# Kernel tuning notes

Hardware: AMD Instinct MI355X
Metric: run time of the kernel (lower is better)

Reference implementation:

```python
import jax, jax.numpy as jnp
import numpy as np

N_NODES = 50000
N_EDGES = 800000
IN_CH = 64
OUT_CH = 32
HEADS = 4
NUM_EDGE_TYPES = 64


def _sincos_pe(max_len, d_model):
    pos = np.arange(max_len, dtype=np.float32)[:, None]
    div = np.exp(np.arange(0, d_model, 2, dtype=np.float32) * (-np.log(10000.0) / d_model))
    pe = np.zeros((max_len, d_model), dtype=np.float32)
    pe[:, 0::2] = np.sin(pos * div)
    pe[:, 1::2] = np.cos(pos * div)
    return jnp.asarray(pe)


def setup_inputs() -> dict:
    key = jax.random.key(0)
    k1, k2, k3, k4, k5, k6 = jax.random.split(key, 6)
    x = jax.random.uniform(k1, (N_NODES, IN_CH), dtype=jnp.float32)
    edge_index = jax.random.randint(k2, (2, N_EDGES), 0, N_NODES, dtype=jnp.int64)
    edge_type = jax.random.randint(k3, (N_EDGES,), 0, NUM_EDGE_TYPES, dtype=jnp.int64)
    pe = _sincos_pe(NUM_EDGE_TYPES, IN_CH)
    W = jax.random.normal(k4, (IN_CH, HEADS * OUT_CH), dtype=jnp.float32) * 0.1
    att_src = jax.random.normal(k5, (HEADS, OUT_CH), dtype=jnp.float32) * 0.1
    att_dst = jax.random.normal(k6, (HEADS, OUT_CH), dtype=jnp.float32) * 0.1
    bias = jnp.zeros((HEADS * OUT_CH,), dtype=jnp.float32)
    return {"x": x, "edge_index": edge_index, "edge_type": edge_type, "pe": pe,
            "W": W, "att_src": att_src, "att_dst": att_dst, "bias": bias}


def reference(x, edge_index, edge_type, pe, W, att_src, att_dst, bias):
    N = x.shape[0]
    H, C = att_src.shape
    src, dst = edge_index[0], edge_index[1]

    # edge-wise positional encoding scatter-added into source nodes
    x_pos = x.at[src].add(pe[edge_type])

    # GATConv (PyG defaults: add_self_loops=True, negative_slope=0.2, concat=True)
    xl = (x_pos @ W).reshape(N, H, C)              # [N, H, C]
    a_src = (xl * att_src[None]).sum(-1)           # [N, H]
    a_dst = (xl * att_dst[None]).sum(-1)           # [N, H]

    self_idx = jnp.arange(N)
    src2 = jnp.concatenate([src, self_idx])        # [E'] with self loops
    dst2 = jnp.concatenate([dst, self_idx])

    alpha = jax.nn.leaky_relu(a_src[src2] + a_dst[dst2], 0.2)   # [E', H]
    amax = jax.ops.segment_max(alpha, dst2, num_segments=N)     # per-target max
    ex = jnp.exp(alpha - amax[dst2])
    denom = jax.ops.segment_sum(ex, dst2, num_segments=N)
    coef = ex / denom[dst2]                                     # segment softmax

    out = jax.ops.segment_sum(coef[:, :, None] * xl[src2], dst2, num_segments=N)
    out = out.reshape(N, H * C) + bias
    return jax.nn.elu(out)
```

## Files before the change

### kernel.cpp

```cpp
#include <hip/hip_runtime.h>
#include <cstdint>
#include <cstddef>

#define N_NODES 50000
#define N_EDGES 800000
#define IN_CH   64
#define OC      128
#define HEADS   4
#define CH      32

#define NB      391
#define BCAP    2560
#define EPB     2048
#define HIST_BLOCKS ((N_EDGES + EPB - 1) / EPB)

#define SENTINEL N_NODES
#define LST_LEN  (N_EDGES + 4 * N_NODES)

typedef __attribute__((ext_vector_type(8))) short short8;
typedef __attribute__((ext_vector_type(4))) float f32x4;

static inline int ceil_div(int a, int b){ return (a + b - 1) / b; }

__device__ __forceinline__ float lrelu(float x){ return fmaxf(x, 0.2f * x); }

__device__ __forceinline__ float bf_lo(unsigned u){ return __uint_as_float(u << 16); }
__device__ __forceinline__ float bf_hi(unsigned u){ return __uint_as_float(u & 0xFFFF0000u); }

__device__ __forceinline__ unsigned pack_bf16(float x, float y){
  unsigned ux = __float_as_uint(x), uy = __float_as_uint(y);
  ux += 0x7FFFu + ((ux >> 16) & 1u);
  uy += 0x7FFFu + ((uy >> 16) & 1u);
  return (ux >> 16) | (uy & 0xFFFF0000u);
}

__global__ __launch_bounds__(256) void k_histA(const int* __restrict__ ei,
                                               const int* __restrict__ et,
                                               int* __restrict__ btail,
                                               unsigned* __restrict__ bbuf){
  __shared__ int cnt[784];
  __shared__ int lofs[784];
  __shared__ int gpos[784];
  __shared__ unsigned stage[2 * EPB];
  __shared__ int sred[256];
  int tid = threadIdx.x;
  for (int i = tid; i < 784; i += 256) cnt[i] = 0;
  __syncthreads();

  int e0 = blockIdx.x * EPB;
  unsigned ent[16];
  int rnk[16];
  short bck[16];
  #pragma unroll
  for (int j = 0; j < 8; ++j){
    int e = e0 + j * 256 + tid;
    bck[2 * j] = -1; bck[2 * j + 1] = -1;
    if (e < N_EDGES){
      int s = ei[e], d = ei[N_EDGES + e], t = et[e];
      int bd = d >> 7, bs = s >> 7;
      ent[2 * j]     = ((unsigned)bd << 23) | ((unsigned)(d & 127) << 16) | (unsigned)s;
      ent[2 * j + 1] = ((unsigned)bs << 23) | ((unsigned)(s & 127) << 16) | (unsigned)t;
      bck[2 * j]     = (short)bd;
      bck[2 * j + 1] = (short)(391 + bs);
      rnk[2 * j]     = atomicAdd(&cnt[bd], 1);
      rnk[2 * j + 1] = atomicAdd(&cnt[391 + bs], 1);
    }
  }
  __syncthreads();

  int v[4], pre[4], run = 0;
  #pragma unroll
  for (int i = 0; i < 4; ++i){
    int idx = tid * 4 + i;
    v[i] = (idx < 784) ? cnt[idx] : 0;
    pre[i] = run; run += v[i];
  }
  sred[tid] = run; __syncthreads();
  for (int off = 1; off < 256; off <<= 1){
    int t = (tid >= off) ? sred[tid - off] : 0;
    __syncthreads();
    sred[tid] += t;
    __syncthreads();
  }
  int toff = sred[tid] - run;
  #pragma unroll
  for (int i = 0; i < 4; ++i){
    int idx = tid * 4 + i;
    if (idx < 784) lofs[idx] = toff + pre[i];
  }
  __syncthreads();

  #pragma unroll
  for (int j = 0; j < 16; ++j){
    if (bck[j] >= 0) stage[lofs[bck[j]] + rnk[j]] = ent[j];
  }
  for (int b = tid; b < 782; b += 256){
    int c = cnt[b];
    gpos[b] = c ? atomicAdd(&btail[b], c) : 0;
  }
  __syncthreads();

  int totalD = lofs[391];
  int totalA = lofs[782];
  for (int i = tid; i < totalA; i += 256){
    unsigned e = stage[i];
    int b9 = (int)(e >> 23);
    int bc = (i < totalD) ? b9 : 391 + b9;
    int gp = gpos[bc] + (i - lofs[bc]);
    if (gp < BCAP) bbuf[(size_t)bc * BCAP + gp] = e;
  }
}

__global__ __launch_bounds__(256) void k_passB(const unsigned* __restrict__ bbuf,
                                               const int* __restrict__ btail,
                                               int* __restrict__ row_dst,
                                               unsigned short* __restrict__ lst,
                                               unsigned* __restrict__ cb){
  int g = blockIdx.x, tid = threadIdx.x;
  if (g < NB){
    __shared__ int cnt[128], sc[128], cur[128], red[256];
    __shared__ int sbase;
    int d0 = g << 7;
    int nn = min(128, N_NODES - d0);
    int cnt_b = min(btail[g], BCAP);
    int part = 0;
    for (int q = tid; q < g; q += 256) part += min(btail[q], BCAP);
    red[tid] = part; __syncthreads();
    for (int off = 128; off > 0; off >>= 1){
      if (tid < off) red[tid] += red[tid + off];
      __syncthreads();
    }
    if (tid == 0) sbase = red[0];
    if (tid < 128) cnt[tid] = 0;
    __syncthreads();
    int base0 = sbase + 4 * d0;
    for (int i = tid; i < cnt_b; i += 256)
      atomicAdd(&cnt[(bbuf[(size_t)g * BCAP + i] >> 16) & 127], 1);
    __syncthreads();
    if (tid < 128) sc[tid] = cnt[tid];
    __syncthreads();
    for (int off = 1; off < 128; off <<= 1){
      int t = (tid < 128 && tid >= off) ? sc[tid - off] : 0;
      __syncthreads();
      if (tid < 128) sc[tid] += t;
      __syncthreads();
    }
    if (tid < nn){
      int ex = sc[tid] - cnt[tid];
      cur[tid] = ex + 4 * tid;
      row_dst[d0 + tid] = base0 + ex + 4 * tid;
    }
    if (g == NB - 1 && tid == 0) row_dst[N_NODES] = base0 + cnt_b + 4 * nn;
    __syncthreads();
    for (int i = tid; i < cnt_b; i += 256){
      unsigned e = bbuf[(size_t)g * BCAP + i];
      int p = atomicAdd(&cur[(e >> 16) & 127], 1);
      lst[base0 + p] = (unsigned short)(e & 0xFFFFu);
    }
    __syncthreads();
    if (tid < nn){
      int pe_ = cur[tid];
      #pragma unroll
      for (int k = 0; k < 4; ++k) lst[base0 + pe_ + k] = (unsigned short)SENTINEL;
    }
  } else {
    __shared__ unsigned hist[128 * 16];
    int n0 = (g - NB) << 7;
    int nn = min(128, N_NODES - n0);
    for (int i = tid; i < 2048; i += 256) hist[i] = 0;
    __syncthreads();
    int cnt_b = min(btail[g], BCAP);
    for (int i = tid; i < cnt_b; i += 256){
      unsigned e = bbuf[(size_t)g * BCAP + i];
      unsigned t = e & 63u;
      atomicAdd(&hist[((e >> 16) & 127) * 16 + (t >> 2)], 1u << (8 * (t & 3)));
    }
    __syncthreads();
    for (int o = tid; o < 4096; o += 256){
      int i = o >> 5, j = o & 31;
      if (i < nn){
        unsigned w = hist[i * 16 + (j >> 1)];
        unsigned sh = 16 * (j & 1);
        cb[(size_t)(n0 + i) * 32 + j] =
          pack_bf16((float)((w >> sh) & 0xFFu), (float)((w >> (sh + 8)) & 0xFFu));
      }
    }
  }
}

__global__ __launch_bounds__(256) void k_prep(const float* __restrict__ pe,
                                              const float* __restrict__ W,
                                              unsigned* __restrict__ Bh,
                                              int* __restrict__ btail,
                                              float* __restrict__ a_src,
                                              unsigned* __restrict__ xh,
                                              unsigned short* __restrict__ lst){
  __shared__ float sPe[64 * 64];
  __shared__ float sW64[64 * 16];
  __shared__ float sPeW[64 * 16];
  int tid = threadIdx.x;
  int nt = blockIdx.x;
  int n0 = nt * 16;
  if (nt == 0){
    for (int i = tid; i < 1024; i += 256) btail[i] = 0;
    if (tid < 64) xh[(size_t)SENTINEL * 64 + tid] = 0;
    if (tid < 4)  a_src[SENTINEL * 4 + tid] = -1e30f;
    if (tid < 32) lst[LST_LEN + tid] = (unsigned short)SENTINEL;
  }
  for (int i = tid; i < 1024; i += 256)
    ((float4*)sPe)[i] = ((const float4*)pe)[i];
  for (int i = tid; i < 1024; i += 256){
    int k = i >> 4, j = i & 15;
    sW64[i] = W[k * 128 + n0 + j];
  }
  __syncthreads();
  for (int i = tid; i < 1024; i += 256){
    int t = i >> 4, j = i & 15;
    float a = 0.f;
    #pragma unroll
    for (int k = 0; k < 64; ++k) a += sPe[t * 64 + k] * sW64[k * 16 + j];
    sPeW[i] = a;
  }
  __syncthreads();
  for (int m = tid; m < 1024; m += 256){
    int j2 = m & 3, l = (m >> 2) & 63, kk = m >> 8;
    int k = kk * 32 + (l >> 4) * 8 + 2 * j2;
    int jl = l & 15;
    float v0, v1;
    if (k < 64){ v0 = sW64[k * 16 + jl]; v1 = sW64[(k + 1) * 16 + jl]; }
    else       { v0 = sPeW[(k - 64) * 16 + jl]; v1 = sPeW[(k - 63) * 16 + jl]; }
    Bh[nt * 1024 + m] = pack_bf16(v0, v1);
  }
}

#define GEMM_ROWS 64
__global__ __launch_bounds__(256) void k_gemm_mfma(const float* __restrict__ x,
                                                   const unsigned* __restrict__ cb,
                                                   const unsigned* __restrict__ Bh,
                                                   const float* __restrict__ att_s,
                                                   const float* __restrict__ att_d,
                                                   float* __restrict__ a_src,
                                                   float* __restrict__ a_dst,
                                                   unsigned* __restrict__ xh){
  __shared__ unsigned sA[4096];
  __shared__ unsigned sB[8192];
  int tid = threadIdx.x;
  int row0 = blockIdx.x * GEMM_ROWS;

  {
    const uint4* srcp = (const uint4*)Bh;
    uint4* dstp = (uint4*)sB;
    #pragma unroll
    for (int i = 0; i < 8; ++i) dstp[tid + i * 256] = srcp[tid + i * 256];
  }
  {
    int r = tid >> 2, q = tid & 3;
    int n = row0 + r;
    unsigned swz = (unsigned)((r & 7) << 4);
    float4 xv[4];
    if (n < N_NODES){
      const float4* xr = (const float4*)(x + (size_t)n * 64);
      #pragma unroll
      for (int i = 0; i < 4; ++i) xv[i] = xr[q * 4 + i];
    } else {
      #pragma unroll
      for (int i = 0; i < 4; ++i) xv[i] = make_float4(0.f, 0.f, 0.f, 0.f);
    }
    unsigned pk[8];
    #pragma unroll
    for (int i = 0; i < 4; ++i){
      pk[2 * i]     = pack_bf16(xv[i].x, xv[i].y);
      pk[2 * i + 1] = pack_bf16(xv[i].z, xv[i].w);
    }
    unsigned b0 = (unsigned)(r * 256 + q * 32);
    *(uint4*)(sA + (((b0)      ^ swz) >> 2)) = make_uint4(pk[0], pk[1], pk[2], pk[3]);
    *(uint4*)(sA + (((b0 + 16) ^ swz) >> 2)) = make_uint4(pk[4], pk[5], pk[6], pk[7]);
    uint4 c0, c1;
    if (n < N_NODES){
      const uint4* cr = (const uint4*)(cb + (size_t)n * 32);
      c0 = cr[q * 2]; c1 = cr[q * 2 + 1];
    } else {
      c0 = make_uint4(0, 0, 0, 0); c1 = c0;
    }
    unsigned b1 = (unsigned)(r * 256 + 128 + q * 32);
    *(uint4*)(sA + (((b1)      ^ swz) >> 2)) = c0;
    *(uint4*)(sA + (((b1 + 16) ^ swz) >> 2)) = c1;
  }
  __syncthreads();

  int wid = tid >> 6, l = tid & 63;
  int c15 = l & 15, kq = l >> 4;
  int arow = wid * 16 + c15;
  f32x4 acc[8];
  #pragma unroll
  for (int nt = 0; nt < 8; ++nt) acc[nt] = (f32x4){0.f, 0.f, 0.f, 0.f};

  #pragma unroll
  for (int kk = 0; kk < 4; ++kk){
    unsigned abyte = (unsigned)(arow * 256 + kk * 64 + kq * 16);
    abyte ^= (unsigned)((arow & 7) << 4);
    short8 af = *(const short8*)((const char*)sA + abyte);
    #pragma unroll
    for (int nt = 0; nt < 8; ++nt){
      short8 bf = *(const short8*)(sB + (size_t)((nt * 4 + kk) * 64 + l) * 4);
      acc[nt] = __builtin_amdgcn_mfma_f32_16x16x32_bf16(af, bf, acc[nt], 0, 0, 0);
    }
  }

  float asv[8], adv[8];
  #pragma unroll
  for (int nt = 0; nt < 8; ++nt){
    asv[nt] = att_s[nt * 16 + c15];
    adv[nt] = att_d[nt * 16 + c15];
  }
  #pragma unroll
  for (int r = 0; r < 4; ++r){
    int row = row0 + wid * 16 + kq * 4 + r;
    bool valid = row < N_NODES;
    #pragma unroll
    for (int h = 0; h < 4; ++h){
      float ps = acc[2 * h][r] * asv[2 * h] + acc[2 * h + 1][r] * asv[2 * h + 1];
      float pd = acc[2 * h][r] * adv[2 * h] + acc[2 * h + 1][r] * adv[2 * h + 1];
      #pragma unroll
      for (int m = 1; m < 16; m <<= 1){
        ps += __shfl_xor(ps, m);
        pd += __shfl_xor(pd, m);
      }
      if (valid && c15 == 0){
        a_src[row * 4 + h] = ps;
        a_dst[row * 4 + h] = pd;
      }
    }
    #pragma unroll
    for (int nt = 0; nt < 8; ++nt){
      float own = acc[nt][r];
      float nb = __shfl_xor(own, 1);
      if (valid && !(c15 & 1))
        xh[(size_t)row * 64 + nt * 8 + (c15 >> 1)] = pack_bf16(own, nb);
    }
  }
}

__global__ __launch_bounds__(256) void k_aggregate(const int* __restrict__ row_dst,
                                                   const unsigned short* __restrict__ lst,
                                                   const float* __restrict__ a_src,
                                                   const float* __restrict__ a_dst,
                                                   const unsigned* __restrict__ xh,
                                                   const float* __restrict__ bias,
                                                   float* __restrict__ out){
  int n = (blockIdx.x * blockDim.x + threadIdx.x) >> 6;
  if (n >= N_NODES) return;
  int l = threadIdx.x & 63;
  int h = l >> 4;
  float ad = a_dst[n * 4 + h];

  float w = __expf(lrelu(a_src[n * 4 + h] + ad));
  unsigned uv = xh[(size_t)n * 64 + l];
  float l0 = w, l1 = 0.f, l2 = 0.f, l3 = 0.f;
  float a0x = w * bf_lo(uv), a0y = w * bf_hi(uv);
  float a1x = 0.f, a1y = 0.f, a2x = 0.f, a2y = 0.f, a3x = 0.f, a3y = 0.f;

  int k0 = row_dst[n];
  int k1 = row_dst[n + 1] - 4;

  int sA = (int)lst[k0], sB = (int)lst[k0 + 1], sC = (int)lst[k0 + 2], sD = (int)lst[k0 + 3];
  unsigned uA = xh[(size_t)sA * 64 + l]; float bA = a_src[sA * 4 + h];
  unsigned uB = xh[(size_t)sB * 64 + l]; float bB = a_src[sB * 4 + h];
  unsigned uC = xh[(size_t)sC * 64 + l]; float bC = a_src[sC * 4 + h];
  unsigned uD = xh[(size_t)sD * 64 + l]; float bD = a_src[sD * 4 + h];

  for (int j = k0; j < k1; j += 4){
    int nsA = (int)lst[j + 4], nsB = (int)lst[j + 5];
    int nsC = (int)lst[j + 6], nsD = (int)lst[j + 7];
    unsigned nuA = xh[(size_t)nsA * 64 + l]; float nbA = a_src[nsA * 4 + h];
    unsigned nuB = xh[(size_t)nsB * 64 + l]; float nbB = a_src[nsB * 4 + h];
    unsigned nuC = xh[(size_t)nsC * 64 + l]; float nbC = a_src[nsC * 4 + h];
    unsigned nuD = xh[(size_t)nsD * 64 + l]; float nbD = a_src[nsD * 4 + h];
    float wA = __expf(lrelu(bA + ad));
    l0 += wA;
    a0x = fmaf(wA, bf_lo(uA), a0x); a0y = fmaf(wA, bf_hi(uA), a0y);
    float wB = __expf(lrelu(bB + ad));
    l1 += wB;
    a1x = fmaf(wB, bf_lo(uB), a1x); a1y = fmaf(wB, bf_hi(uB), a1y);
    float wC = __expf(lrelu(bC + ad));
    l2 += wC;
    a2x = fmaf(wC, bf_lo(uC), a2x); a2y = fmaf(wC, bf_hi(uC), a2y);
    float wD = __expf(lrelu(bD + ad));
    l3 += wD;
    a3x = fmaf(wD, bf_lo(uD), a3x); a3y = fmaf(wD, bf_hi(uD), a3y);
    uA = nuA; bA = nbA; uB = nuB; bB = nbB;
    uC = nuC; bC = nbC; uD = nuD; bD = nbD;
  }
  float lsum = (l0 + l1) + (l2 + l3);
  float accx = (a0x + a1x) + (a2x + a3x);
  float accy = (a0y + a1y) + (a2y + a3y);
  float2 b = ((const float2*)bias)[l];
  float r0 = accx / lsum + b.x;
  float r1 = accy / lsum + b.y;
  float2 o;
  o.x = r0 > 0.f ? r0 : expm1f(r0);
  o.y = r1 > 0.f ? r1 : expm1f(r1);
  ((float2*)out)[(size_t)n * 64 + l] = o;
}

extern "C" void kernel_launch(void* const* d_in, const int* in_sizes, int n_in,
                              void* d_out, int out_size, void* d_ws, size_t ws_size,
                              hipStream_t stream){
  const float* x     = (const float*)d_in[0];
  const int*   ei    = (const int*)d_in[1];
  const int*   et    = (const int*)d_in[2];
  const float* pe    = (const float*)d_in[3];
  const float* W     = (const float*)d_in[4];
  const float* att_s = (const float*)d_in[5];
  const float* att_d = (const float*)d_in[6];
  const float* bias  = (const float*)d_in[7];
  float* out = (float*)d_out;

  int*      btail   = (int*)d_ws;
  int*      row_dst = btail + 1024;
  unsigned* Bh      = (unsigned*)(row_dst + N_NODES + 8);
  unsigned* cb      = Bh + 8192;
  float*    a_src   = (float*)(cb + (size_t)N_NODES * 32);
  float*    a_dst   = a_src + (size_t)(N_NODES + 1) * 4;
  unsigned* xh      = (unsigned*)(a_dst + (size_t)N_NODES * 4);
  unsigned* bbuf    = xh + (size_t)(N_NODES + 1) * 64;
  unsigned short* lst = (unsigned short*)(bbuf + (size_t)2 * NB * BCAP);

  const int B = 256;

  k_prep<<<8, B, 0, stream>>>(pe, W, Bh, btail, a_src, xh, lst);
  k_histA<<<HIST_BLOCKS, B, 0, stream>>>(ei, et, btail, bbuf);
  k_passB<<<2 * NB, B, 0, stream>>>(bbuf, btail, row_dst, lst, cb);
  k_gemm_mfma<<<ceil_div(N_NODES, GEMM_ROWS), B, 0, stream>>>(x, cb, Bh,
                                                              att_s, att_d,
                                                              a_src, a_dst, xh);
  k_aggregate<<<ceil_div(N_NODES * 64, B), B, 0, stream>>>(row_dst, lst, a_src, a_dst,
                                                           xh, bias, out);
}
```

Before: 105.5 us.

## Fuse edge-type histogram and MFMA GEMM into passB source-bucket blocks

The source-bucket half of k_passB now runs the bf16 MFMA projection directly from its shared-memory edge-type histogram, in two 64-row halves per 128-node bucket. This drops the cb count matrix round trip through global memory and the separate k_gemm_mfma launch. In exchange, those blocks use much more shared memory (about 56KB), which may lower occupancy, and they now do the GEMM serially after the histogram.

```diff
diff --git a/kernel.cpp b/kernel.cpp
--- a/kernel.cpp
+++ b/kernel.cpp
@@ -115,7 +115,13 @@
                                                const int* __restrict__ btail,
                                                int* __restrict__ row_dst,
                                                unsigned short* __restrict__ lst,
-                                               unsigned* __restrict__ cb){
+                                               const float* __restrict__ x,
+                                               const unsigned* __restrict__ Bh,
+                                               const float* __restrict__ att_s,
+                                               const float* __restrict__ att_d,
+                                               float* __restrict__ a_src,
+                                               float* __restrict__ a_dst,
+                                               unsigned* __restrict__ xh){
   int g = blockIdx.x, tid = threadIdx.x;
   if (g < NB){
     __shared__ int cnt[128], sc[128], cur[128], red[256];
@@ -165,8 +171,9 @@
     }
   } else {
     __shared__ unsigned hist[128 * 16];
+    __shared__ unsigned sB[8192];
+    __shared__ unsigned sA[4096];
     int n0 = (g - NB) << 7;
-    int nn = min(128, N_NODES - n0);
     for (int i = tid; i < 2048; i += 256) hist[i] = 0;
     __syncthreads();
     int cnt_b = min(btail[g], BCAP);
@@ -175,15 +182,106 @@
       unsigned t = e & 63u;
       atomicAdd(&hist[((e >> 16) & 127) * 16 + (t >> 2)], 1u << (8 * (t & 3)));
     }
-    __syncthreads();
-    for (int o = tid; o < 4096; o += 256){
-      int i = o >> 5, j = o & 31;
-      if (i < nn){
-        unsigned w = hist[i * 16 + (j >> 1)];
-        unsigned sh = 16 * (j & 1);
-        cb[(size_t)(n0 + i) * 32 + j] =
-          pack_bf16((float)((w >> sh) & 0xFFu), (float)((w >> (sh + 8)) & 0xFFu));
+    {
+      const uint4* srcp = (const uint4*)Bh;
+      uint4* dstp = (uint4*)sB;
+      #pragma unroll
+      for (int i = 0; i < 8; ++i) dstp[tid + i * 256] = srcp[tid + i * 256];
+    }
+    __syncthreads();
+
+    int wid = tid >> 6, l = tid & 63;
+    int c15 = l & 15, kq = l >> 4;
+    float asv[8], adv[8];
+    #pragma unroll
+    for (int nt = 0; nt < 8; ++nt){
+      asv[nt] = att_s[nt * 16 + c15];
+      adv[nt] = att_d[nt * 16 + c15];
+    }
+
+    for (int half = 0; half < 2; ++half){
+      int row0 = n0 + half * 64;
+      {
+        int r = tid >> 2, q = tid & 3;
+        int n = row0 + r;
+        unsigned swz = (unsigned)((r & 7) << 4);
+        float4 xv[4];
+        if (n < N_NODES){
+          const float4* xr = (const float4*)(x + (size_t)n * 64);
+          #pragma unroll
+          for (int i = 0; i < 4; ++i) xv[i] = xr[q * 4 + i];
+        } else {
+          #pragma unroll
+          for (int i = 0; i < 4; ++i) xv[i] = make_float4(0.f, 0.f, 0.f, 0.f);
+        }
+        unsigned pk[8];
+        #pragma unroll
+        for (int i = 0; i < 4; ++i){
+          pk[2 * i]     = pack_bf16(xv[i].x, xv[i].y);
+          pk[2 * i + 1] = pack_bf16(xv[i].z, xv[i].w);
+        }
+        unsigned b0 = (unsigned)(r * 256 + q * 32);
+        *(uint4*)(sA + (((b0)      ^ swz) >> 2)) = make_uint4(pk[0], pk[1], pk[2], pk[3]);
+        *(uint4*)(sA + (((b0 + 16) ^ swz) >> 2)) = make_uint4(pk[4], pk[5], pk[6], pk[7]);
+        unsigned cw[4];
+        #pragma unroll
+        for (int i = 0; i < 4; ++i) cw[i] = hist[(half * 64 + r) * 16 + q * 4 + i];
+        unsigned pc[8];
+        #pragma unroll
+        for (int i = 0; i < 4; ++i){
+          unsigned w = cw[i];
+          pc[2 * i]     = pack_bf16((float)(w & 0xFFu), (float)((w >> 8) & 0xFFu));
+          pc[2 * i + 1] = pack_bf16((float)((w >> 16) & 0xFFu), (float)(w >> 24));
+        }
+        unsigned b1 = (unsigned)(r * 256 + 128 + q * 32);
+        *(uint4*)(sA + (((b1)      ^ swz) >> 2)) = make_uint4(pc[0], pc[1], pc[2], pc[3]);
+        *(uint4*)(sA + (((b1 + 16) ^ swz) >> 2)) = make_uint4(pc[4], pc[5], pc[6], pc[7]);
       }
+      __syncthreads();
+
+      int arow = wid * 16 + c15;
+      f32x4 acc[8];
+      #pragma unroll
+      for (int nt = 0; nt < 8; ++nt) acc[nt] = (f32x4){0.f, 0.f, 0.f, 0.f};
+      #pragma unroll
+      for (int kk = 0; kk < 4; ++kk){
+        unsigned abyte = (unsigned)(arow * 256 + kk * 64 + kq * 16);
+        abyte ^= (unsigned)((arow & 7) << 4);
+        short8 af = *(const short8*)((const char*)sA + abyte);
+        #pragma unroll
+        for (int nt = 0; nt < 8; ++nt){
+          short8 bf = *(const short8*)(sB + (size_t)((nt * 4 + kk) * 64 + l) * 4);
+          acc[nt] = __builtin_amdgcn_mfma_f32_16x16x32_bf16(af, bf, acc[nt], 0, 0, 0);
+        }
+      }
+
+      #pragma unroll
+      for (int r = 0; r < 4; ++r){
+        int row = row0 + wid * 16 + kq * 4 + r;
+        bool valid = row < N_NODES;
+        #pragma unroll
+        for (int h = 0; h < 4; ++h){
+          float ps = acc[2 * h][r] * asv[2 * h] + acc[2 * h + 1][r] * asv[2 * h + 1];
+          float pd = acc[2 * h][r] * adv[2 * h] + acc[2 * h + 1][r] * adv[2 * h + 1];
+          #pragma unroll
+          for (int m = 1; m < 16; m <<= 1){
+            ps += __shfl_xor(ps, m);
+            pd += __shfl_xor(pd, m);
+          }
+          if (valid && c15 == 0){
+            a_src[row * 4 + h] = ps;
+            a_dst[row * 4 + h] = pd;
+          }
+        }
+        #pragma unroll
+        for (int nt = 0; nt < 8; ++nt){
+          float own = acc[nt][r];
+          float nb = __shfl_xor(own, 1);
+          if (valid && !(c15 & 1))
+            xh[(size_t)row * 64 + nt * 8 + (c15 >> 1)] = pack_bf16(own, nb);
+        }
+      }
+      __syncthreads();
     }
   }
 }
@@ -230,114 +328,6 @@
     if (k < 64){ v0 = sW64[k * 16 + jl]; v1 = sW64[(k + 1) * 16 + jl]; }
     else       { v0 = sPeW[(k - 64) * 16 + jl]; v1 = sPeW[(k - 63) * 16 + jl]; }
     Bh[nt * 1024 + m] = pack_bf16(v0, v1);
-  }
-}
-
-#define GEMM_ROWS 64
-__global__ __launch_bounds__(256) void k_gemm_mfma(const float* __restrict__ x,
-                                                   const unsigned* __restrict__ cb,
-                                                   const unsigned* __restrict__ Bh,
-                                                   const float* __restrict__ att_s,
-                                                   const float* __restrict__ att_d,
-                                                   float* __restrict__ a_src,
-                                                   float* __restrict__ a_dst,
-                                                   unsigned* __restrict__ xh){
-  __shared__ unsigned sA[4096];
-  __shared__ unsigned sB[8192];
-  int tid = threadIdx.x;
-  int row0 = blockIdx.x * GEMM_ROWS;
-
-  {
-    const uint4* srcp = (const uint4*)Bh;
-    uint4* dstp = (uint4*)sB;
-    #pragma unroll
-    for (int i = 0; i < 8; ++i) dstp[tid + i * 256] = srcp[tid + i * 256];
-  }
-  {
-    int r = tid >> 2, q = tid & 3;
-    int n = row0 + r;
-    unsigned swz = (unsigned)((r & 7) << 4);
-    float4 xv[4];
-    if (n < N_NODES){
-      const float4* xr = (const float4*)(x + (size_t)n * 64);
-      #pragma unroll
-      for (int i = 0; i < 4; ++i) xv[i] = xr[q * 4 + i];
-    } else {
-      #pragma unroll
-      for (int i = 0; i < 4; ++i) xv[i] = make_float4(0.f, 0.f, 0.f, 0.f);
-    }
-    unsigned pk[8];
-    #pragma unroll
-    for (int i = 0; i < 4; ++i){
-      pk[2 * i]     = pack_bf16(xv[i].x, xv[i].y);
-      pk[2 * i + 1] = pack_bf16(xv[i].z, xv[i].w);
-    }
-    unsigned b0 = (unsigned)(r * 256 + q * 32);
-    *(uint4*)(sA + (((b0)      ^ swz) >> 2)) = make_uint4(pk[0], pk[1], pk[2], pk[3]);
-    *(uint4*)(sA + (((b0 + 16) ^ swz) >> 2)) = make_uint4(pk[4], pk[5], pk[6], pk[7]);
-    uint4 c0, c1;
-    if (n < N_NODES){
-      const uint4* cr = (const uint4*)(cb + (size_t)n * 32);
-      c0 = cr[q * 2]; c1 = cr[q * 2 + 1];
-    } else {
-      c0 = make_uint4(0, 0, 0, 0); c1 = c0;
-    }
-    unsigned b1 = (unsigned)(r * 256 + 128 + q * 32);
-    *(uint4*)(sA + (((b1)      ^ swz) >> 2)) = c0;
-    *(uint4*)(sA + (((b1 + 16) ^ swz) >> 2)) = c1;
-  }
-  __syncthreads();
-
-  int wid = tid >> 6, l = tid & 63;
-  int c15 = l & 15, kq = l >> 4;
-  int arow = wid * 16 + c15;
-  f32x4 acc[8];
-  #pragma unroll
-  for (int nt = 0; nt < 8; ++nt) acc[nt] = (f32x4){0.f, 0.f, 0.f, 0.f};
-
-  #pragma unroll
-  for (int kk = 0; kk < 4; ++kk){
-    unsigned abyte = (unsigned)(arow * 256 + kk * 64 + kq * 16);
-    abyte ^= (unsigned)((arow & 7) << 4);
-    short8 af = *(const short8*)((const char*)sA + abyte);
-    #pragma unroll
-    for (int nt = 0; nt < 8; ++nt){
-      short8 bf = *(const short8*)(sB + (size_t)((nt * 4 + kk) * 64 + l) * 4);
-      acc[nt] = __builtin_amdgcn_mfma_f32_16x16x32_bf16(af, bf, acc[nt], 0, 0, 0);
-    }
-  }
-
-  float asv[8], adv[8];
-  #pragma unroll
-  for (int nt = 0; nt < 8; ++nt){
-    asv[nt] = att_s[nt * 16 + c15];
-    adv[nt] = att_d[nt * 16 + c15];
-  }
-  #pragma unroll
-  for (int r = 0; r < 4; ++r){
-    int row = row0 + wid * 16 + kq * 4 + r;
-    bool valid = row < N_NODES;
-    #pragma unroll
-    for (int h = 0; h < 4; ++h){
-      float ps = acc[2 * h][r] * asv[2 * h] + acc[2 * h + 1][r] * asv[2 * h + 1];
-      float pd = acc[2 * h][r] * adv[2 * h] + acc[2 * h + 1][r] * adv[2 * h + 1];
-      #pragma unroll
-      for (int m = 1; m < 16; m <<= 1){
-        ps += __shfl_xor(ps, m);
-        pd += __shfl_xor(pd, m);
-      }
-      if (valid && c15 == 0){
-        a_src[row * 4 + h] = ps;
-        a_dst[row * 4 + h] = pd;
-      }
-    }
-    #pragma unroll
-    for (int nt = 0; nt < 8; ++nt){
-      float own = acc[nt][r];
-      float nb = __shfl_xor(own, 1);
-      if (valid && !(c15 & 1))
-        xh[(size_t)row * 64 + nt * 8 + (c15 >> 1)] = pack_bf16(own, nb);
-    }
   }
 }
 
@@ -419,8 +409,7 @@
   int*      btail   = (int*)d_ws;
   int*      row_dst = btail + 1024;
   unsigned* Bh      = (unsigned*)(row_dst + N_NODES + 8);
-  unsigned* cb      = Bh + 8192;
-  float*    a_src   = (float*)(cb + (size_t)N_NODES * 32);
+  float*    a_src   = (float*)(Bh + 8192);
   float*    a_dst   = a_src + (size_t)(N_NODES + 1) * 4;
   unsigned* xh      = (unsigned*)(a_dst + (size_t)N_NODES * 4);
   unsigned* bbuf    = xh + (size_t)(N_NODES + 1) * 64;
@@ -430,10 +419,8 @@
 
   k_prep<<<8, B, 0, stream>>>(pe, W, Bh, btail, a_src, xh, lst);
   k_histA<<<HIST_BLOCKS, B, 0, stream>>>(ei, et, btail, bbuf);
-  k_passB<<<2 * NB, B, 0, stream>>>(bbuf, btail, row_dst, lst, cb);
-  k_gemm_mfma<<<ceil_div(N_NODES, GEMM_ROWS), B, 0, stream>>>(x, cb, Bh,
-                                                              att_s, att_d,
-                                                              a_src, a_dst, xh);
+  k_passB<<<2 * NB, B, 0, stream>>>(bbuf, btail, row_dst, lst,
+                                    x, Bh, att_s, att_d, a_src, a_dst, xh);
   k_aggregate<<<ceil_div(N_NODES * 64, B), B, 0, stream>>>(row_dst, lst, a_src, a_dst,
                                                            xh, bias, out);
 }
```

Measured after the change: 103.0 us. -2.4%, faster.
